# Performance work log

Hardware: AMD Instinct MI355X
Metric: run time of the kernel (lower is better)

## Reference

```python
import jax, jax.numpy as jnp
import numpy as np

RMS_EPS = 1e-6

def rms_norm(x, w, eps=RMS_EPS):
    # LLaMA RMSNorm: x * rsqrt(mean(x^2) + eps) * w
    var = jnp.mean(jnp.square(x), axis=-1, keepdims=True)
    return x * jax.lax.rsqrt(var + eps) * w

def setup_inputs() -> dict:
    key = jax.random.key(0)
    k1, k2, k3 = jax.random.split(key, 3)
    B, S, D, V = 2, 2048, 4096, 32000
    hidden_states = jax.random.normal(k1, (B, S, D), dtype=jnp.float32)
    norm_weight = jnp.ones((D,), dtype=jnp.float32)
    lm_head_weight = jax.random.normal(k2, (V, D), dtype=jnp.float32) * 0.02
    attention_mask = jnp.ones((B, S), dtype=jnp.int32)
    labels = jax.random.randint(k3, (B, S), 0, V, dtype=jnp.int32).astype(jnp.int64)
    return {
        "hidden_states": hidden_states,
        "norm_weight": norm_weight,
        "lm_head_weight": lm_head_weight,
        "attention_mask": attention_mask,
        "labels": labels,
    }

def reference(hidden_states, norm_weight, lm_head_weight, attention_mask, labels):
    B, S, D = hidden_states.shape
    V = lm_head_weight.shape[0]
    h = rms_norm(hidden_states, norm_weight)
    # lm_head: Linear(D -> V, bias=False); cast logits to fp32 (full-vocab tensor)
    logits = jnp.einsum('bsd,vd->bsv', h, lm_head_weight).astype(jnp.float32)
    # shift: drop last logit position / first label position.
    # attention_mask is all-ones here, so the boolean select keeps every row
    # -> static-shape flatten to [B*(S-1), V], matching torch semantics.
    shift_logits = logits[:, :-1, :].reshape(B * (S - 1), V)
    shift_labels = labels[:, 1:].reshape(B * (S - 1))
    return shift_logits, shift_labels
```

## Files before the change

### kernel.cpp

```cpp
#include <hip/hip_runtime.h>
#include <hip/hip_bf16.h>
#include <stdint.h>

#define B_DIM 2
#define S_DIM 2048
#define D_DIM 4096
#define V_DIM 32000
#define M_DIM (B_DIM * S_DIM)
#define OUT_ROWS (B_DIM * (S_DIM-1))

typedef __hip_bfloat16 bf16;
typedef __bf16 bf16x8 __attribute__((ext_vector_type(8)));
typedef float floatx4 __attribute__((ext_vector_type(4)));

__device__ __forceinline__ void async16(const bf16* g, bf16* l) {
    __builtin_amdgcn_global_load_lds(
        (const __attribute__((address_space(1))) void*)g,
        (__attribute__((address_space(3))) void*)l,
        16, 0, 0);
}

__global__ void rmsnorm_cast_kernel(const float* __restrict__ x,
                                    const float* __restrict__ w,
                                    bf16* __restrict__ h) {
    const int row = blockIdx.x;
    const int t = threadIdx.x;
    const float* xr = x + (size_t)row * D_DIM;

    float4 vals[4];
    float ss = 0.f;
#pragma unroll
    for (int i = 0; i < 4; ++i) {
        float4 v = ((const float4*)xr)[t + i * 256];
        vals[i] = v;
        ss += v.x * v.x + v.y * v.y + v.z * v.z + v.w * v.w;
    }
#pragma unroll
    for (int off = 32; off; off >>= 1) ss += __shfl_down(ss, off, 64);
    __shared__ float wsum[4];
    const int lane = t & 63, wv = t >> 6;
    if (lane == 0) wsum[wv] = ss;
    __syncthreads();
    const float var = (wsum[0] + wsum[1] + wsum[2] + wsum[3]) * (1.0f / D_DIM);
    const float scale = rsqrtf(var + 1e-6f);

    bf16* hr = h + (size_t)row * D_DIM;
#pragma unroll
    for (int i = 0; i < 4; ++i) {
        const int f4 = t + i * 256;
        float4 v = vals[i];
        float4 wv4 = ((const float4*)w)[f4];
        ushort4 pk;
        bf16 b0 = __float2bfloat16(v.x * scale * wv4.x);
        bf16 b1 = __float2bfloat16(v.y * scale * wv4.y);
        bf16 b2 = __float2bfloat16(v.z * scale * wv4.z);
        bf16 b3 = __float2bfloat16(v.w * scale * wv4.w);
        pk.x = *(unsigned short*)&b0;
        pk.y = *(unsigned short*)&b1;
        pk.z = *(unsigned short*)&b2;
        pk.w = *(unsigned short*)&b3;
        ((ushort4*)hr)[f4] = pk;
    }
}

__global__ void wcast_kernel(const float* __restrict__ W, bf16* __restrict__ Wb) {
    const size_t i = (size_t)blockIdx.x * 256 + threadIdx.x;
    float4 v = ((const float4*)W)[i];
    ushort4 pk;
    bf16 b0 = __float2bfloat16(v.x);
    bf16 b1 = __float2bfloat16(v.y);
    bf16 b2 = __float2bfloat16(v.z);
    bf16 b3 = __float2bfloat16(v.w);
    pk.x = *(unsigned short*)&b0;
    pk.y = *(unsigned short*)&b1;
    pk.z = *(unsigned short*)&b2;
    pk.w = *(unsigned short*)&b3;
    ((ushort4*)Wb)[i] = pk;
}

#define BM 128
#define BN 128
#define BK 32

__global__ __launch_bounds__(256) void gemm_kernel(const bf16* __restrict__ A,
                                                   const bf16* __restrict__ Bw,
                                                   float* __restrict__ Cout) {
    __shared__ __align__(16) bf16 As[BM * BK];
    __shared__ __align__(16) bf16 Bs[BN * BK];

    const int bid = blockIdx.x;
    const int bm = bid & 31;
    const int bn = bid >> 5;
    const int m0 = bm * BM;
    const int n0 = bn * BN;

    const int t = threadIdx.x;
    const int lane = t & 63;
    const int wv = t >> 6;
    const int wm = (wv & 1) * 64;
    const int wn = (wv >> 1) * 64;
    const int quad = lane >> 4;
    const int l15 = lane & 15;

    floatx4 acc[4][4] = {};

    const int gi0 = t;
    const int gi1 = t + 256;

    for (int kt = 0; kt < D_DIM / BK; ++kt) {
        const int k0 = kt * BK;
        {
            const int row0 = gi0 >> 2, kc0 = (gi0 & 3) * 8;
            const int row1 = gi1 >> 2, kc1 = (gi1 & 3) * 8;
            async16(&A[(size_t)(m0 + row0) * D_DIM + k0 + kc0], &As[gi0 * 8]);
            async16(&A[(size_t)(m0 + row1) * D_DIM + k0 + kc1], &As[gi1 * 8]);
            async16(&Bw[(size_t)(n0 + row0) * D_DIM + k0 + kc0], &Bs[gi0 * 8]);
            async16(&Bw[(size_t)(n0 + row1) * D_DIM + k0 + kc1], &Bs[gi1 * 8]);
        }
        __syncthreads();

        bf16x8 af[4], bfr[4];
#pragma unroll
        for (int i = 0; i < 4; ++i) {
            af[i]  = *(const bf16x8*)&As[(wm + i * 16 + l15) * BK + quad * 8];
            bfr[i] = *(const bf16x8*)&Bs[(wn + i * 16 + l15) * BK + quad * 8];
        }
#pragma unroll
        for (int mi = 0; mi < 4; ++mi)
#pragma unroll
            for (int ni = 0; ni < 4; ++ni)
                acc[mi][ni] = __builtin_amdgcn_mfma_f32_16x16x32_bf16(
                    af[mi], bfr[ni], acc[mi][ni], 0, 0, 0);
        __syncthreads();
    }

#pragma unroll
    for (int mi = 0; mi < 4; ++mi) {
#pragma unroll
        for (int r = 0; r < 4; ++r) {
            const int m = m0 + wm + mi * 16 + quad * 4 + r;
            const int s = m & (S_DIM - 1);
            if (s == S_DIM - 1) continue;
            const int orow = (m >> 11) * (S_DIM - 1) + s;
            float* cp = Cout + (size_t)orow * V_DIM + n0 + wn;
#pragma unroll
            for (int ni = 0; ni < 4; ++ni)
                cp[ni * 16 + l15] = acc[mi][ni][r];
        }
    }
}

__global__ void labels_kernel(const int* __restrict__ labels, float* __restrict__ out) {
    const int r = blockIdx.x * 256 + threadIdx.x;
    if (r >= OUT_ROWS) return;
    const int b = r / (S_DIM - 1);
    const int s = r % (S_DIM - 1);
    out[r] = (float)labels[b * S_DIM + s + 1];
}

extern "C" void kernel_launch(void* const* d_in, const int* in_sizes, int n_in,
                              void* d_out, int out_size, void* d_ws, size_t ws_size,
                              hipStream_t stream) {
    const float* x      = (const float*)d_in[0];
    const float* nw     = (const float*)d_in[1];
    const float* W      = (const float*)d_in[2];
    const int*   labels = (const int*)d_in[4];

    float* logits_out = (float*)d_out;
    float* labels_out = logits_out + (size_t)OUT_ROWS * V_DIM;

    bf16* h  = (bf16*)d_ws;
    bf16* Wb = h + (size_t)M_DIM * D_DIM;

    rmsnorm_cast_kernel<<<M_DIM, 256, 0, stream>>>(x, nw, h);
    wcast_kernel<<<(int)((size_t)V_DIM * D_DIM / 4 / 256), 256, 0, stream>>>(W, Wb);
    gemm_kernel<<<32 * (V_DIM / BN), 256, 0, stream>>>(h, Wb, logits_out);
    labels_kernel<<<(OUT_ROWS + 255) / 256, 256, 0, stream>>>(labels, labels_out);
}
```

Baseline: 2.525 ms.

## Rewrite GEMM with 256x256 tiles, double-buffered LDS, swizzle and interleaved prefetch

The bf16 GEMM moves from 128x128x32 tiles with 4 waves to 256x256x64 tiles with 8 waves. It double-buffers LDS and issues async global-to-LDS prefetches between MFMA phases, with explicit vmcnt waits and s_setprio around the MFMA bursts. An XOR swizzle on LDS columns avoids bank conflicts, and a block-index remap groups XCD work. This targets the low arithmetic intensity and exposed load latency of the old single-buffered loop, at the cost of 128KB of LDS, higher register pressure and delicate barrier/wait ordering.

```diff
diff --git a/kernel.cpp b/kernel.cpp
--- a/kernel.cpp
+++ b/kernel.cpp
@@ -78,74 +78,154 @@
     ((ushort4*)Wb)[i] = pk;
 }
 
-#define BM 128
-#define BN 128
-#define BK 32
-
-__global__ __launch_bounds__(256) void gemm_kernel(const bf16* __restrict__ A,
-                                                   const bf16* __restrict__ Bw,
-                                                   float* __restrict__ Cout) {
-    __shared__ __align__(16) bf16 As[BM * BK];
-    __shared__ __align__(16) bf16 Bs[BN * BK];
+#define BM 256
+#define BN 256
+#define BK 64
+
+#define STAGE_A(db, half, kt) do { \
+    const bf16* _g = aRow0 + (size_t)(half) * 128 * D_DIM + (kt) * BK; \
+    bf16* _l = lds + (db) * 32768 + (half) * 8192 + t * 8; \
+    async16(_g, _l); \
+    async16(_g + (size_t)64 * D_DIM, _l + 4096); \
+} while (0)
+
+#define STAGE_B(db, half, kt) do { \
+    const bf16* _g = bRow0 + (size_t)(half) * 128 * D_DIM + (kt) * BK; \
+    bf16* _l = lds + (db) * 32768 + 16384 + (half) * 8192 + t * 8; \
+    async16(_g, _l); \
+    async16(_g + (size_t)64 * D_DIM, _l + 4096); \
+} while (0)
+
+#define LDA(db, mi, ks) (*(const bf16x8*)(lds + (db) * 32768 + aBase + (mi) * 1024 + ((ks) ? csw1 : csw0)))
+#define LDB(db, ni, ks) (*(const bf16x8*)(lds + (db) * 32768 + bBase + (ni) * 1024 + ((ks) ? csw1 : csw0)))
+#define MFMA(a, b, c) __builtin_amdgcn_mfma_f32_16x16x32_bf16((a), (b), (c), 0, 0, 0)
+#define BAR() __builtin_amdgcn_s_barrier()
+#define PRIO1() __builtin_amdgcn_s_setprio(1)
+#define PRIO0() __builtin_amdgcn_s_setprio(0)
+
+__global__ __launch_bounds__(512, 2) void gemm_kernel(const bf16* __restrict__ A,
+                                                      const bf16* __restrict__ Bw,
+                                                      float* __restrict__ Cout) {
+    __shared__ __align__(16) bf16 lds[65536];
 
     const int bid = blockIdx.x;
-    const int bm = bid & 31;
-    const int bn = bid >> 5;
-    const int m0 = bm * BM;
-    const int n0 = bn * BN;
-
-    const int t = threadIdx.x;
+    const int wg  = (bid & 7) * 250 + (bid >> 3);
+    const int bm  = wg & 15;
+    const int bn  = wg >> 4;
+    const int m0  = bm * BM, n0 = bn * BN;
+
+    const int t    = threadIdx.x;
     const int lane = t & 63;
-    const int wv = t >> 6;
-    const int wm = (wv & 1) * 64;
-    const int wn = (wv >> 1) * 64;
+    const int wv   = t >> 6;
+    const int wmi  = wv >> 2;
+    const int wni  = wv & 3;
     const int quad = lane >> 4;
-    const int l15 = lane & 15;
-
-    floatx4 acc[4][4] = {};
-
-    const int gi0 = t;
-    const int gi1 = t + 256;
-
-    for (int kt = 0; kt < D_DIM / BK; ++kt) {
-        const int k0 = kt * BK;
-        {
-            const int row0 = gi0 >> 2, kc0 = (gi0 & 3) * 8;
-            const int row1 = gi1 >> 2, kc1 = (gi1 & 3) * 8;
-            async16(&A[(size_t)(m0 + row0) * D_DIM + k0 + kc0], &As[gi0 * 8]);
-            async16(&A[(size_t)(m0 + row1) * D_DIM + k0 + kc1], &As[gi1 * 8]);
-            async16(&Bw[(size_t)(n0 + row0) * D_DIM + k0 + kc0], &Bs[gi0 * 8]);
-            async16(&Bw[(size_t)(n0 + row1) * D_DIM + k0 + kc1], &Bs[gi1 * 8]);
+    const int l15  = lane & 15;
+
+    const int r0 = t >> 3;
+    const int c0 = ((t & 7) ^ (r0 & 7)) << 3;
+    const bf16* aRow0 = A  + (size_t)(m0 + r0) * D_DIM + c0;
+    const bf16* bRow0 = Bw + (size_t)(n0 + r0) * D_DIM + c0;
+
+    const int vx   = (l15 & 7) << 3;
+    const int csw0 = ((quad << 3)     ) ^ vx;
+    const int csw1 = ((quad << 3) | 32) ^ vx;
+    const int aBase = wmi * 8192 + l15 * 64;
+    const int bBase = 16384 + (wni >> 1) * 8192 + (wni & 1) * 4096 + l15 * 64;
+
+    floatx4 acc[8][4] = {};
+    bf16x8 af[4][2], b01[2][2], b23[2][2];
+
+    STAGE_B(0, 0, 0); STAGE_B(0, 1, 0); STAGE_A(0, 0, 0); STAGE_A(0, 1, 0);
+    STAGE_B(1, 0, 1); STAGE_B(1, 1, 1); STAGE_A(1, 0, 1); STAGE_A(1, 1, 1);
+    asm volatile("s_waitcnt vmcnt(8)" ::: "memory");
+    BAR();
+
+    for (int it = 0; it < 32; ++it) {
+        int kta = 2 * it + 2; if (kta > 63) kta = 63;
+        int ktb = 2 * it + 3; if (ktb > 63) ktb = 63;
+
+#pragma unroll
+        for (int db = 0; db < 2; ++db) {
+#pragma unroll
+            for (int mi = 0; mi < 4; ++mi) { af[mi][0] = LDA(db, mi, 0); af[mi][1] = LDA(db, mi, 1); }
+#pragma unroll
+            for (int ni = 0; ni < 2; ++ni) { b01[ni][0] = LDB(db, ni, 0); b01[ni][1] = LDB(db, ni, 1); }
+            if (db == 1) STAGE_A(0, 0, kta);
+            BAR();
+            PRIO1();
+#pragma unroll
+            for (int mi = 0; mi < 4; ++mi)
+#pragma unroll
+                for (int ni = 0; ni < 2; ++ni) {
+                    acc[mi][ni] = MFMA(af[mi][0], b01[ni][0], acc[mi][ni]);
+                    acc[mi][ni] = MFMA(af[mi][1], b01[ni][1], acc[mi][ni]);
+                }
+            PRIO0();
+            BAR();
+
+#pragma unroll
+            for (int ni = 0; ni < 2; ++ni) { b23[ni][0] = LDB(db, ni + 2, 0); b23[ni][1] = LDB(db, ni + 2, 1); }
+            if (db == 1) STAGE_A(0, 1, kta);
+            BAR();
+            PRIO1();
+#pragma unroll
+            for (int mi = 0; mi < 4; ++mi)
+#pragma unroll
+                for (int ni = 0; ni < 2; ++ni) {
+                    acc[mi][ni + 2] = MFMA(af[mi][0], b23[ni][0], acc[mi][ni + 2]);
+                    acc[mi][ni + 2] = MFMA(af[mi][1], b23[ni][1], acc[mi][ni + 2]);
+                }
+            PRIO0();
+            BAR();
+
+#pragma unroll
+            for (int mi = 0; mi < 4; ++mi) { af[mi][0] = LDA(db, mi + 4, 0); af[mi][1] = LDA(db, mi + 4, 1); }
+            if (db == 0) { STAGE_B(0, 0, kta); }
+            else         { STAGE_B(1, 0, ktb); STAGE_B(1, 1, ktb); }
+            BAR();
+            PRIO1();
+#pragma unroll
+            for (int mi = 0; mi < 4; ++mi)
+#pragma unroll
+                for (int ni = 0; ni < 2; ++ni) {
+                    acc[mi + 4][ni] = MFMA(af[mi][0], b01[ni][0], acc[mi + 4][ni]);
+                    acc[mi + 4][ni] = MFMA(af[mi][1], b01[ni][1], acc[mi + 4][ni]);
+                }
+            PRIO0();
+            BAR();
+
+            if (db == 0) { STAGE_B(0, 1, kta); }
+            else         { STAGE_A(1, 0, ktb); STAGE_A(1, 1, ktb); }
+            BAR();
+            PRIO1();
+#pragma unroll
+            for (int mi = 0; mi < 4; ++mi)
+#pragma unroll
+                for (int ni = 0; ni < 2; ++ni) {
+                    acc[mi + 4][ni + 2] = MFMA(af[mi][0], b23[ni][0], acc[mi + 4][ni + 2]);
+                    acc[mi + 4][ni + 2] = MFMA(af[mi][1], b23[ni][1], acc[mi + 4][ni + 2]);
+                }
+            PRIO0();
+            if (db == 0) { asm volatile("s_waitcnt vmcnt(4)" ::: "memory"); }
+            else         { asm volatile("s_waitcnt vmcnt(8)" ::: "memory"); }
+            BAR();
         }
-        __syncthreads();
-
-        bf16x8 af[4], bfr[4];
-#pragma unroll
-        for (int i = 0; i < 4; ++i) {
-            af[i]  = *(const bf16x8*)&As[(wm + i * 16 + l15) * BK + quad * 8];
-            bfr[i] = *(const bf16x8*)&Bs[(wn + i * 16 + l15) * BK + quad * 8];
-        }
-#pragma unroll
-        for (int mi = 0; mi < 4; ++mi)
-#pragma unroll
-            for (int ni = 0; ni < 4; ++ni)
-                acc[mi][ni] = __builtin_amdgcn_mfma_f32_16x16x32_bf16(
-                    af[mi], bfr[ni], acc[mi][ni], 0, 0, 0);
-        __syncthreads();
-    }
-
-#pragma unroll
-    for (int mi = 0; mi < 4; ++mi) {
+    }
+
+    const int mbase = m0 + wmi * 128 + quad * 4;
+    const int nbase = n0 + wni * 64 + l15;
+#pragma unroll
+    for (int mi = 0; mi < 8; ++mi) {
 #pragma unroll
         for (int r = 0; r < 4; ++r) {
-            const int m = m0 + wm + mi * 16 + quad * 4 + r;
+            const int m = mbase + mi * 16 + r;
             const int s = m & (S_DIM - 1);
             if (s == S_DIM - 1) continue;
-            const int orow = (m >> 11) * (S_DIM - 1) + s;
-            float* cp = Cout + (size_t)orow * V_DIM + n0 + wn;
+            float* cp = Cout + (size_t)((m >> 11) * (S_DIM - 1) + s) * V_DIM + nbase;
 #pragma unroll
             for (int ni = 0; ni < 4; ++ni)
-                cp[ni * 16 + l15] = acc[mi][ni][r];
+                cp[ni * 16] = acc[mi][ni][r];
         }
     }
 }
@@ -174,6 +254,6 @@
 
     rmsnorm_cast_kernel<<<M_DIM, 256, 0, stream>>>(x, nw, h);
     wcast_kernel<<<(int)((size_t)V_DIM * D_DIM / 4 / 256), 256, 0, stream>>>(W, Wb);
-    gemm_kernel<<<32 * (V_DIM / BN), 256, 0, stream>>>(h, Wb, logits_out);
+    gemm_kernel<<<(M_DIM / BM) * (V_DIM / BN), 512, 0, stream>>>(h, Wb, logits_out);
     labels_kernel<<<(OUT_ROWS + 255) / 256, 256, 0, stream>>>(labels, labels_out);
 }
```

Measured after the change: 2.328 ms. 1.08x faster.
